# Kernel optimization log

Measured on AMD Instinct MI355X. Metric: run time of the kernel, lower is better.

Reference implementation:

```python
import jax, jax.numpy as jnp
import numpy as np
import math

D_MODEL = 1024
N_HEADS = 16
D_K = D_MODEL // N_HEADS
B, S = 2, 2048


def setup_inputs() -> dict:
    key = jax.random.key(0)
    ks = jax.random.split(key, 11)
    sc = 1.0 / math.sqrt(D_MODEL)
    inp = {
        'q': jax.random.normal(ks[0], (B, S, D_MODEL), jnp.float32),
        'k': jax.random.normal(ks[1], (B, S, D_MODEL), jnp.float32),
        'v': jax.random.normal(ks[2], (B, S, D_MODEL), jnp.float32),
        'mask': jnp.tril(jnp.ones((S, S), jnp.int32))[None, None],  # [1,1,S,S] causal
        'W_q': jax.random.normal(ks[3], (D_MODEL, D_MODEL), jnp.float32) * sc,
        'b_q': jnp.zeros((D_MODEL,), jnp.float32),
        'W_k': jax.random.normal(ks[4], (D_MODEL, D_MODEL), jnp.float32) * sc,
        'b_k': jnp.zeros((D_MODEL,), jnp.float32),
        'W_v': jax.random.normal(ks[5], (D_MODEL, D_MODEL), jnp.float32) * sc,
        'b_v': jnp.zeros((D_MODEL,), jnp.float32),
        'W_o': jax.random.normal(ks[6], (D_MODEL, D_MODEL), jnp.float32) * sc,
        'b_o': jnp.zeros((D_MODEL,), jnp.float32),
    }
    return inp


def reference(q, k, v, mask, W_q, b_q, W_k, b_k, W_v, b_v, W_o, b_o):
    # Linear projections then split heads: [B,S,D] -> [B,H,S,d_k]
    def split_heads(x):
        b, s, _ = x.shape
        return x.reshape(b, s, N_HEADS, D_K).transpose(0, 2, 1, 3)

    Q = split_heads(q @ W_q + b_q)
    K = split_heads(k @ W_k + b_k)
    V = split_heads(v @ W_v + b_v)

    scores = jnp.einsum('bhqd,bhkd->bhqk', Q, K) / math.sqrt(D_K)
    scores = jnp.where(mask == 0, jnp.float32(-1e9), scores)
    attn = jax.nn.softmax(scores, axis=-1)  # dropout is identity in eval mode
    out = jnp.einsum('bhqk,bhkd->bhqd', attn, V)
    out = out.transpose(0, 2, 1, 3).reshape(q.shape[0], -1, D_MODEL)
    return out @ W_o + b_o
```

## Files before the change

kernel.cpp:

```cpp
#include <hip/hip_runtime.h>
#include <hip/hip_bf16.h>

#define D_MODEL 1024
#define S_LEN   2048
#define BATCH   2
#define NH      16
#define DK      64

typedef __bf16 bf16_t;
typedef __attribute__((ext_vector_type(8))) __bf16 bf16x8;
typedef __attribute__((ext_vector_type(4))) float f32x4;

#if __has_builtin(__builtin_amdgcn_exp2f)
#define EXP2F(x) __builtin_amdgcn_exp2f(x)
#else
#define EXP2F(x) exp2f(x)
#endif

#define Q_SCALE 0.1803368801111204f

#define GLDS16(gp, lp) __builtin_amdgcn_global_load_lds( \
    (const __attribute__((address_space(1))) void*)(gp), \
    (__attribute__((address_space(3))) void*)(lp), 16, 0, 0)

__global__ __launch_bounds__(256) void cvt_qkv(const float* __restrict__ q,
                                               const float* __restrict__ k,
                                               const float* __restrict__ v,
                                               bf16_t* __restrict__ out) {
    const long NELEM = (long)BATCH * S_LEN * D_MODEL;
    const float* src = (blockIdx.y == 0) ? q : (blockIdx.y == 1) ? k : v;
    long i = ((long)blockIdx.x * 256 + threadIdx.x) * 8;
    float4 a = *(const float4*)(src + i);
    float4 b = *(const float4*)(src + i + 4);
    bf16x8 o;
    o[0] = (bf16_t)a.x; o[1] = (bf16_t)a.y; o[2] = (bf16_t)a.z; o[3] = (bf16_t)a.w;
    o[4] = (bf16_t)b.x; o[5] = (bf16_t)b.y; o[6] = (bf16_t)b.z; o[7] = (bf16_t)b.w;
    *(bf16x8*)(out + blockIdx.y * NELEM + i) = o;
}

__global__ void wt_transpose4(const float* __restrict__ Wq, const float* __restrict__ Wk,
                              const float* __restrict__ Wv, const float* __restrict__ Wo,
                              bf16_t* __restrict__ WqkvT, bf16_t* __restrict__ WoT) {
    __shared__ float t[32][33];
    const float* in = (blockIdx.z == 0) ? Wq : (blockIdx.z == 1) ? Wk
                    : (blockIdx.z == 2) ? Wv : Wo;
    bf16_t* out = (blockIdx.z < 3) ? (WqkvT + (long)blockIdx.z * D_MODEL * D_MODEL) : WoT;
    int tx = threadIdx.x, ty = threadIdx.y;
    int gx = blockIdx.x * 32, gy = blockIdx.y * 32;
#pragma unroll
    for (int i = 0; i < 32; i += 8)
        t[ty + i][tx] = in[(gy + ty + i) * D_MODEL + gx + tx];
    __syncthreads();
#pragma unroll
    for (int i = 0; i < 32; i += 8)
        out[(gx + ty + i) * D_MODEL + gy + tx] = (bf16_t)t[tx][ty + i];
}

__global__ void v_transpose(const bf16_t* __restrict__ in, bf16_t* __restrict__ out) {
    __shared__ bf16_t t[32][33];
    int tx = threadIdx.x, ty = threadIdx.y;
    int bh = blockIdx.z;
    int s0 = blockIdx.x * 32, d0 = blockIdx.y * 32;
    const bf16_t* ip = in + (long)bh * S_LEN * DK;
    bf16_t* op = out + (long)bh * DK * S_LEN;
#pragma unroll
    for (int i = 0; i < 32; i += 8)
        t[ty + i][tx] = ip[(long)(s0 + ty + i) * DK + d0 + tx];
    __syncthreads();
#pragma unroll
    for (int i = 0; i < 32; i += 8)
        op[(long)(d0 + ty + i) * S_LEN + s0 + tx] = t[tx][ty + i];
}

#define BM 128
#define BN 128
#define BKT 64

__device__ __forceinline__ void swizzle_xy(int bx, int by, int& n0, int& m0) {
    int lin = by * 8 + bx;
    n0 = (lin >> 5) * BN;
    m0 = (lin & 31) * BM;
}

__device__ __forceinline__ void stage_swz(const bf16_t* __restrict__ G, int row0,
                                          int k0, bf16_t* __restrict__ Ls, int tid) {
#pragma unroll
    for (int it = 0; it < 4; ++it) {
        int g = it * 256 + tid;
        int row = g >> 3;
        int c = (g & 7) ^ (row & 7);
        GLDS16(&G[(long)(row0 + row) * D_MODEL + k0 + c * 8],
               &Ls[(it * 256 + (tid & ~63)) * 8]);
    }
}

__device__ __forceinline__ bf16x8 frag_swz(const bf16_t* __restrict__ Ls, int row, int cg) {
    return *(const bf16x8*)(&Ls[(row * 8 + (cg ^ (row & 7))) * 8]);
}

__global__ __launch_bounds__(256) void gemm_qkv(
    const bf16_t* __restrict__ qkvb, const bf16_t* __restrict__ WqkvT,
    const float* __restrict__ bq, const float* __restrict__ bk, const float* __restrict__ bv,
    bf16_t* __restrict__ Qw, bf16_t* __restrict__ Kw, bf16_t* __restrict__ Vw)
{
    __shared__ __align__(16) bf16_t As[BM * BKT];
    __shared__ __align__(16) bf16_t Bs[BN * BKT];
    const int z = blockIdx.z;
    const bf16_t* A  = qkvb + (long)z * BATCH * S_LEN * D_MODEL;
    const bf16_t* BT = WqkvT + (long)z * D_MODEL * D_MODEL;
    const float* bias = (z == 0) ? bq : (z == 1) ? bk : bv;
    bf16_t* Cb = (z == 0) ? Qw : (z == 1) ? Kw : Vw;
    const float oscale = (z == 0) ? Q_SCALE : 1.0f;

    const int tid  = threadIdx.x;
    const int wave = tid >> 6, lane = tid & 63;
    const int lrow = lane & 15, kgrp = lane >> 4;
    const int wm = (wave >> 1) * 64, wn = (wave & 1) * 64;
    int m0, n0;
    swizzle_xy(blockIdx.x, blockIdx.y, n0, m0);

    f32x4 acc[4][4] = {};

    for (int k0 = 0; k0 < D_MODEL; k0 += BKT) {
        stage_swz(A, m0, k0, As, tid);
        stage_swz(BT, n0, k0, Bs, tid);
        __syncthreads();
#pragma unroll
        for (int kk = 0; kk < 2; ++kk) {
            bf16x8 af[4], bfr[4];
#pragma unroll
            for (int mi = 0; mi < 4; ++mi)
                af[mi] = frag_swz(As, wm + mi * 16 + lrow, kk * 4 + kgrp);
#pragma unroll
            for (int ni = 0; ni < 4; ++ni)
                bfr[ni] = frag_swz(Bs, wn + ni * 16 + lrow, kk * 4 + kgrp);
#pragma unroll
            for (int mi = 0; mi < 4; ++mi)
#pragma unroll
                for (int ni = 0; ni < 4; ++ni)
                    acc[mi][ni] = __builtin_amdgcn_mfma_f32_16x16x32_bf16(af[mi], bfr[ni], acc[mi][ni], 0, 0, 0);
        }
        __syncthreads();
    }

#pragma unroll
    for (int mi = 0; mi < 4; ++mi)
#pragma unroll
        for (int ni = 0; ni < 4; ++ni) {
            int col = n0 + wn + ni * 16 + lrow;
            float bvf = bias[col];
#pragma unroll
            for (int r = 0; r < 4; ++r) {
                int row = m0 + wm + mi * 16 + kgrp * 4 + r;
                float vv = (acc[mi][ni][r] + bvf) * oscale;
                int b = row >> 11, s = row & (S_LEN - 1);
                int h = col >> 6, d = col & (DK - 1);
                Cb[(((long)(b * NH + h) * S_LEN + s) * DK) + d] = (bf16_t)vv;
            }
        }
}

__global__ __launch_bounds__(256) void gemm_out(
    const bf16_t* __restrict__ A, const bf16_t* __restrict__ BT,
    const float* __restrict__ bias, float* __restrict__ Cf)
{
    __shared__ __align__(16) bf16_t As[BM * BKT];
    __shared__ __align__(16) bf16_t Bs[BN * BKT];
    const int tid  = threadIdx.x;
    const int wave = tid >> 6, lane = tid & 63;
    const int lrow = lane & 15, kgrp = lane >> 4;
    const int wm = (wave >> 1) * 64, wn = (wave & 1) * 64;
    int m0, n0;
    swizzle_xy(blockIdx.x, blockIdx.y, n0, m0);

    f32x4 acc[4][4] = {};

    for (int k0 = 0; k0 < D_MODEL; k0 += BKT) {
        stage_swz(A, m0, k0, As, tid);
        stage_swz(BT, n0, k0, Bs, tid);
        __syncthreads();
#pragma unroll
        for (int kk = 0; kk < 2; ++kk) {
            bf16x8 af[4], bfr[4];
#pragma unroll
            for (int mi = 0; mi < 4; ++mi)
                af[mi] = frag_swz(As, wm + mi * 16 + lrow, kk * 4 + kgrp);
#pragma unroll
            for (int ni = 0; ni < 4; ++ni)
                bfr[ni] = frag_swz(Bs, wn + ni * 16 + lrow, kk * 4 + kgrp);
#pragma unroll
            for (int mi = 0; mi < 4; ++mi)
#pragma unroll
                for (int ni = 0; ni < 4; ++ni)
                    acc[mi][ni] = __builtin_amdgcn_mfma_f32_16x16x32_bf16(af[mi], bfr[ni], acc[mi][ni], 0, 0, 0);
        }
        __syncthreads();
    }

#pragma unroll
    for (int mi = 0; mi < 4; ++mi)
#pragma unroll
        for (int ni = 0; ni < 4; ++ni) {
            int col = n0 + wn + ni * 16 + lrow;
            float bvf = bias[col];
#pragma unroll
            for (int r = 0; r < 4; ++r) {
                int row = m0 + wm + mi * 16 + kgrp * 4 + r;
                Cf[(long)row * D_MODEL + col] = acc[mi][ni][r] + bvf;
            }
        }
}

__global__ __launch_bounds__(256, 5) void attn_kernel(
    const bf16_t* __restrict__ Q, const bf16_t* __restrict__ K,
    const bf16_t* __restrict__ Vt, bf16_t* __restrict__ O)
{
    __shared__ __align__(16) bf16_t Ks[64 * 72];
    __shared__ __align__(16) bf16_t Vs[64 * 72];
    __shared__ __align__(16) bf16_t Ps[4][16 * 72];

    const int bh = blockIdx.y;
    const int qi = gridDim.x - 1 - blockIdx.x;
    const int q0 = qi * 64;
    const int tid = threadIdx.x, wave = tid >> 6, lane = tid & 63;
    const int lrow = lane & 15, kgrp = lane >> 4;
    const int qrow = q0 + wave * 16;

    const bf16_t* Qh  = Q  + (long)bh * S_LEN * DK;
    const bf16_t* Kh  = K  + (long)bh * S_LEN * DK;
    const bf16_t* Vth = Vt + (long)bh * DK * S_LEN;

    const int f0 = tid * 8;
    const int r0 = f0 >> 6, c0 = f0 & 63;
    const int r1 = (f0 + 2048) >> 6;

    bf16x8 qf[2];
#pragma unroll
    for (int kk = 0; kk < 2; ++kk)
        qf[kk] = *(const bf16x8*)(&Qh[(qrow + lrow) * DK + kk * 32 + kgrp * 8]);

    f32x4 acc[4] = {};
    float lsum[4] = {0.f, 0.f, 0.f, 0.f};

    const int nt = qi + 1;

    uint4 kpre0 = *(const uint4*)(&Kh[(long)r0 * DK + c0]);
    uint4 kpre1 = *(const uint4*)(&Kh[(long)r1 * DK + c0]);
    uint4 vpre0 = *(const uint4*)(&Vth[(long)r0 * S_LEN + c0]);
    uint4 vpre1 = *(const uint4*)(&Vth[(long)r1 * S_LEN + c0]);

    for (int t = 0; t < nt; ++t) {
        __syncthreads();
        *(uint4*)(&Ks[r0 * 72 + c0]) = kpre0;
        *(uint4*)(&Ks[r1 * 72 + c0]) = kpre1;
        *(uint4*)(&Vs[r0 * 72 + c0]) = vpre0;
        *(uint4*)(&Vs[r1 * 72 + c0]) = vpre1;
        if (t + 1 < nt) {
            const int j0n = (t + 1) * 64;
            kpre0 = *(const uint4*)(&Kh[(long)(j0n + r0) * DK + c0]);
            kpre1 = *(const uint4*)(&Kh[(long)(j0n + r1) * DK + c0]);
            vpre0 = *(const uint4*)(&Vth[(long)r0 * S_LEN + j0n + c0]);
            vpre1 = *(const uint4*)(&Vth[(long)r1 * S_LEN + j0n + c0]);
        }
        __syncthreads();

        const int j0 = t * 64;

        f32x4 sc[4] = {};
#pragma unroll
        for (int kk = 0; kk < 2; ++kk)
#pragma unroll
            for (int ni = 0; ni < 4; ++ni) {
                bf16x8 kf = *(const bf16x8*)(&Ks[(ni * 16 + lrow) * 72 + kk * 32 + kgrp * 8]);
                sc[ni] = __builtin_amdgcn_mfma_f32_16x16x32_bf16(qf[kk], kf, sc[ni], 0, 0, 0);
            }

        const bool needmask = (j0 + 63 > qrow);
        if (needmask) {
#pragma unroll
            for (int r = 0; r < 4; ++r) {
                int row = qrow + kgrp * 4 + r;
#pragma unroll
                for (int ni = 0; ni < 4; ++ni) {
                    int colj = j0 + ni * 16 + lrow;
                    float pv = EXP2F(sc[ni][r]);
                    if (colj > row) pv = 0.f;
                    lsum[r] += pv;
                    Ps[wave][(kgrp * 4 + r) * 72 + ni * 16 + lrow] = (bf16_t)pv;
                }
            }
        } else {
#pragma unroll
            for (int r = 0; r < 4; ++r)
#pragma unroll
                for (int ni = 0; ni < 4; ++ni) {
                    float pv = EXP2F(sc[ni][r]);
                    lsum[r] += pv;
                    Ps[wave][(kgrp * 4 + r) * 72 + ni * 16 + lrow] = (bf16_t)pv;
                }
        }

#pragma unroll
        for (int kk = 0; kk < 2; ++kk) {
            bf16x8 pf = *(const bf16x8*)(&Ps[wave][lrow * 72 + kk * 32 + kgrp * 8]);
#pragma unroll
            for (int di = 0; di < 4; ++di) {
                bf16x8 vf = *(const bf16x8*)(&Vs[(di * 16 + lrow) * 72 + kk * 32 + kgrp * 8]);
                acc[di] = __builtin_amdgcn_mfma_f32_16x16x32_bf16(pf, vf, acc[di], 0, 0, 0);
            }
        }
    }

#pragma unroll
    for (int r = 0; r < 4; ++r)
#pragma unroll
        for (int off = 1; off < 16; off <<= 1)
            lsum[r] += __shfl_xor(lsum[r], off);

    const int b = bh >> 4, h = bh & (NH - 1);
#pragma unroll
    for (int r = 0; r < 4; ++r) {
        int s = qrow + kgrp * 4 + r;
        float inv = 1.f / lsum[r];
#pragma unroll
        for (int di = 0; di < 4; ++di) {
            int d = di * 16 + lrow;
            O[((long)(b * S_LEN + s)) * D_MODEL + h * DK + d] = (bf16_t)(acc[di][r] * inv);
        }
    }
}

extern "C" void kernel_launch(void* const* d_in, const int* in_sizes, int n_in,
                              void* d_out, int out_size, void* d_ws, size_t ws_size,
                              hipStream_t stream) {
    const float* q  = (const float*)d_in[0];
    const float* k  = (const float*)d_in[1];
    const float* v  = (const float*)d_in[2];
    const float* Wq = (const float*)d_in[4];
    const float* bq = (const float*)d_in[5];
    const float* Wk = (const float*)d_in[6];
    const float* bk = (const float*)d_in[7];
    const float* Wv = (const float*)d_in[8];
    const float* bv = (const float*)d_in[9];
    const float* Wo = (const float*)d_in[10];
    const float* bo = (const float*)d_in[11];

    char* ws = (char*)d_ws;
    const size_t Mi = 1024 * 1024;
    bf16_t* WqkvT = (bf16_t*)(ws);
    bf16_t* WoT   = (bf16_t*)(ws + 6 * Mi);
    bf16_t* Qw    = (bf16_t*)(ws + 8 * Mi);
    bf16_t* Kw    = (bf16_t*)(ws + 16 * Mi);
    bf16_t* Vw    = (bf16_t*)(ws + 24 * Mi);
    bf16_t* qkvb  = (bf16_t*)(ws + 32 * Mi);
    bf16_t* Vtw   = (bf16_t*)(ws + 32 * Mi);
    bf16_t* Aw    = (bf16_t*)(ws + 40 * Mi);

    const long NELEM = (long)BATCH * S_LEN * D_MODEL;
    cvt_qkv<<<dim3((int)(NELEM / 2048), 3), 256, 0, stream>>>(q, k, v, qkvb);

    dim3 tb(32, 8);
    wt_transpose4<<<dim3(D_MODEL / 32, D_MODEL / 32, 4), tb, 0, stream>>>(
        Wq, Wk, Wv, Wo, WqkvT, WoT);

    gemm_qkv<<<dim3(D_MODEL / BN, (BATCH * S_LEN) / BM, 3), 256, 0, stream>>>(
        qkvb, WqkvT, bq, bk, bv, Qw, Kw, Vw);

    v_transpose<<<dim3(S_LEN / 32, DK / 32, BATCH * NH), tb, 0, stream>>>(Vw, Vtw);

    attn_kernel<<<dim3(S_LEN / 64, BATCH * NH), 256, 0, stream>>>(Qw, Kw, Vtw, Aw);

    gemm_out<<<dim3(D_MODEL / BN, (BATCH * S_LEN) / BM), 256, 0, stream>>>(
        Aw, WoT, bo, (float*)d_out);
}
```

Baseline: 264.2 us.

## Split causal attention over key chunks with atomic fp32 accumulation

```diff
diff --git a/kernel.cpp b/kernel.cpp
--- a/kernel.cpp
+++ b/kernel.cpp
@@ -211,16 +211,30 @@
         }
 }
 
+__global__ __launch_bounds__(256) void zero_acc(float* __restrict__ Oacc,
+                                                float* __restrict__ Lacc) {
+    f32x4 z = {0.f, 0.f, 0.f, 0.f};
+    int b = blockIdx.x;
+    if (b < 4096)
+        *(f32x4*)(&Oacc[((long)b * 256 + threadIdx.x) * 4]) = z;
+    else
+        *(f32x4*)(&Lacc[((long)(b - 4096) * 256 + threadIdx.x) * 4]) = z;
+}
+
 __global__ __launch_bounds__(256, 5) void attn_kernel(
     const bf16_t* __restrict__ Q, const bf16_t* __restrict__ K,
-    const bf16_t* __restrict__ Vt, bf16_t* __restrict__ O)
+    const bf16_t* __restrict__ Vt, float* __restrict__ Oacc,
+    float* __restrict__ Lacc)
 {
+    const int ci = blockIdx.x, qi = blockIdx.y, bh = blockIdx.z;
+    const int t0 = ci * 8;
+    if (t0 > qi) return;
+    const int t1 = min(t0 + 8, qi + 1);
+
     __shared__ __align__(16) bf16_t Ks[64 * 72];
     __shared__ __align__(16) bf16_t Vs[64 * 72];
     __shared__ __align__(16) bf16_t Ps[4][16 * 72];
 
-    const int bh = blockIdx.y;
-    const int qi = gridDim.x - 1 - blockIdx.x;
     const int q0 = qi * 64;
     const int tid = threadIdx.x, wave = tid >> 6, lane = tid & 63;
     const int lrow = lane & 15, kgrp = lane >> 4;
@@ -242,20 +256,19 @@
     f32x4 acc[4] = {};
     float lsum[4] = {0.f, 0.f, 0.f, 0.f};
 
-    const int nt = qi + 1;
-
-    uint4 kpre0 = *(const uint4*)(&Kh[(long)r0 * DK + c0]);
-    uint4 kpre1 = *(const uint4*)(&Kh[(long)r1 * DK + c0]);
-    uint4 vpre0 = *(const uint4*)(&Vth[(long)r0 * S_LEN + c0]);
-    uint4 vpre1 = *(const uint4*)(&Vth[(long)r1 * S_LEN + c0]);
-
-    for (int t = 0; t < nt; ++t) {
+    const int j00 = t0 * 64;
+    uint4 kpre0 = *(const uint4*)(&Kh[(long)(j00 + r0) * DK + c0]);
+    uint4 kpre1 = *(const uint4*)(&Kh[(long)(j00 + r1) * DK + c0]);
+    uint4 vpre0 = *(const uint4*)(&Vth[(long)r0 * S_LEN + j00 + c0]);
+    uint4 vpre1 = *(const uint4*)(&Vth[(long)r1 * S_LEN + j00 + c0]);
+
+    for (int t = t0; t < t1; ++t) {
         __syncthreads();
         *(uint4*)(&Ks[r0 * 72 + c0]) = kpre0;
         *(uint4*)(&Ks[r1 * 72 + c0]) = kpre1;
         *(uint4*)(&Vs[r0 * 72 + c0]) = vpre0;
         *(uint4*)(&Vs[r1 * 72 + c0]) = vpre1;
-        if (t + 1 < nt) {
+        if (t + 1 < t1) {
             const int j0n = (t + 1) * 64;
             kpre0 = *(const uint4*)(&Kh[(long)(j0n + r0) * DK + c0]);
             kpre1 = *(const uint4*)(&Kh[(long)(j0n + r1) * DK + c0]);
@@ -317,17 +330,37 @@
         for (int off = 1; off < 16; off <<= 1)
             lsum[r] += __shfl_xor(lsum[r], off);
 
-    const int b = bh >> 4, h = bh & (NH - 1);
 #pragma unroll
     for (int r = 0; r < 4; ++r) {
-        int s = qrow + kgrp * 4 + r;
-        float inv = 1.f / lsum[r];
-#pragma unroll
-        for (int di = 0; di < 4; ++di) {
-            int d = di * 16 + lrow;
-            O[((long)(b * S_LEN + s)) * D_MODEL + h * DK + d] = (bf16_t)(acc[di][r] * inv);
-        }
+        int q = qrow + kgrp * 4 + r;
+        float* orow = &Oacc[((long)bh * S_LEN + q) * DK];
+#pragma unroll
+        for (int di = 0; di < 4; ++di)
+            unsafeAtomicAdd(&orow[di * 16 + lrow], acc[di][r]);
+        if (lrow == 0)
+            unsafeAtomicAdd(&Lacc[bh * S_LEN + q], lsum[r]);
     }
+}
+
+__global__ __launch_bounds__(256) void attn_norm(const float* __restrict__ Oacc,
+                                                 const float* __restrict__ Lacc,
+                                                 bf16_t* __restrict__ Aw) {
+    long i8 = ((long)blockIdx.x * 256 + threadIdx.x) * 8;
+    int row = (int)(i8 >> 10);
+    int col = (int)(i8 & 1023);
+    int b = row >> 11, s = row & (S_LEN - 1);
+    int h = col >> 6, d = col & (DK - 1);
+    int bh = b * NH + h;
+    float inv = 1.f / Lacc[bh * S_LEN + s];
+    const float* src = &Oacc[((long)bh * S_LEN + s) * DK + d];
+    float4 a = *(const float4*)src;
+    float4 c = *(const float4*)(src + 4);
+    bf16x8 o;
+    o[0] = (bf16_t)(a.x * inv); o[1] = (bf16_t)(a.y * inv);
+    o[2] = (bf16_t)(a.z * inv); o[3] = (bf16_t)(a.w * inv);
+    o[4] = (bf16_t)(c.x * inv); o[5] = (bf16_t)(c.y * inv);
+    o[6] = (bf16_t)(c.z * inv); o[7] = (bf16_t)(c.w * inv);
+    *(bf16x8*)(&Aw[i8]) = o;
 }
 
 extern "C" void kernel_launch(void* const* d_in, const int* in_sizes, int n_in,
@@ -354,7 +387,9 @@
     bf16_t* Vw    = (bf16_t*)(ws + 24 * Mi);
     bf16_t* qkvb  = (bf16_t*)(ws + 32 * Mi);
     bf16_t* Vtw   = (bf16_t*)(ws + 32 * Mi);
-    bf16_t* Aw    = (bf16_t*)(ws + 40 * Mi);
+    float*  Oacc  = (float*) (ws + 40 * Mi);
+    float*  Lacc  = (float*) (ws);
+    bf16_t* Aw    = (bf16_t*)(ws + 24 * Mi);
 
     const long NELEM = (long)BATCH * S_LEN * D_MODEL;
     cvt_qkv<<<dim3((int)(NELEM / 2048), 3), 256, 0, stream>>>(q, k, v, qkvb);
@@ -368,7 +403,12 @@
 
     v_transpose<<<dim3(S_LEN / 32, DK / 32, BATCH * NH), tb, 0, stream>>>(Vw, Vtw);
 
-    attn_kernel<<<dim3(S_LEN / 64, BATCH * NH), 256, 0, stream>>>(Qw, Kw, Vtw, Aw);
+    zero_acc<<<4160, 256, 0, stream>>>(Oacc, Lacc);
+
+    attn_kernel<<<dim3(8, S_LEN / 64, BATCH * NH), 256, 0, stream>>>(
+        Qw, Kw, Vtw, Oacc, Lacc);
+
+    attn_norm<<<(int)(NELEM / 2048), 256, 0, stream>>>(Oacc, Lacc, Aw);
 
     gemm_out<<<dim3(D_MODEL / BN, (BATCH * S_LEN) / BM), 256, 0, stream>>>(
         Aw, WoT, bo, (float*)d_out);
```

Measured after the change: 326.2 us. +23.5%, slower.

## Split attention KV loop across two wave groups with LDS reduction

Applied to the files above, without the earlier changes.

```diff
diff --git a/kernel.cpp b/kernel.cpp
--- a/kernel.cpp
+++ b/kernel.cpp
@@ -211,20 +211,22 @@
         }
 }
 
-__global__ __launch_bounds__(256, 5) void attn_kernel(
+__global__ __launch_bounds__(512, 4) void attn_kernel(
     const bf16_t* __restrict__ Q, const bf16_t* __restrict__ K,
     const bf16_t* __restrict__ Vt, bf16_t* __restrict__ O)
 {
-    __shared__ __align__(16) bf16_t Ks[64 * 72];
-    __shared__ __align__(16) bf16_t Vs[64 * 72];
-    __shared__ __align__(16) bf16_t Ps[4][16 * 72];
+    __shared__ __align__(16) bf16_t Ka[64 * 72], Va[64 * 72];
+    __shared__ __align__(16) bf16_t Kb[64 * 72], Vb[64 * 72];
+    __shared__ __align__(16) bf16_t Ps[8][16 * 72];
+    __shared__ float Ms[4 * 64 * 20];
 
     const int bh = blockIdx.y;
     const int qi = gridDim.x - 1 - blockIdx.x;
     const int q0 = qi * 64;
     const int tid = threadIdx.x, wave = tid >> 6, lane = tid & 63;
+    const int grp = wave >> 2, w4 = wave & 3;
     const int lrow = lane & 15, kgrp = lane >> 4;
-    const int qrow = q0 + wave * 16;
+    const int qrow = q0 + w4 * 16;
 
     const bf16_t* Qh  = Q  + (long)bh * S_LEN * DK;
     const bf16_t* Kh  = K  + (long)bh * S_LEN * DK;
@@ -232,7 +234,6 @@
 
     const int f0 = tid * 8;
     const int r0 = f0 >> 6, c0 = f0 & 63;
-    const int r1 = (f0 + 2048) >> 6;
 
     bf16x8 qf[2];
 #pragma unroll
@@ -243,89 +244,119 @@
     float lsum[4] = {0.f, 0.f, 0.f, 0.f};
 
     const int nt = qi + 1;
-
-    uint4 kpre0 = *(const uint4*)(&Kh[(long)r0 * DK + c0]);
-    uint4 kpre1 = *(const uint4*)(&Kh[(long)r1 * DK + c0]);
-    uint4 vpre0 = *(const uint4*)(&Vth[(long)r0 * S_LEN + c0]);
-    uint4 vpre1 = *(const uint4*)(&Vth[(long)r1 * S_LEN + c0]);
-
-    for (int t = 0; t < nt; ++t) {
-        __syncthreads();
-        *(uint4*)(&Ks[r0 * 72 + c0]) = kpre0;
-        *(uint4*)(&Ks[r1 * 72 + c0]) = kpre1;
-        *(uint4*)(&Vs[r0 * 72 + c0]) = vpre0;
-        *(uint4*)(&Vs[r1 * 72 + c0]) = vpre1;
-        if (t + 1 < nt) {
-            const int j0n = (t + 1) * 64;
-            kpre0 = *(const uint4*)(&Kh[(long)(j0n + r0) * DK + c0]);
-            kpre1 = *(const uint4*)(&Kh[(long)(j0n + r1) * DK + c0]);
-            vpre0 = *(const uint4*)(&Vth[(long)r0 * S_LEN + j0n + c0]);
-            vpre1 = *(const uint4*)(&Vth[(long)r1 * S_LEN + j0n + c0]);
-        }
-        __syncthreads();
-
-        const int j0 = t * 64;
-
-        f32x4 sc[4] = {};
-#pragma unroll
-        for (int kk = 0; kk < 2; ++kk)
-#pragma unroll
-            for (int ni = 0; ni < 4; ++ni) {
-                bf16x8 kf = *(const bf16x8*)(&Ks[(ni * 16 + lrow) * 72 + kk * 32 + kgrp * 8]);
-                sc[ni] = __builtin_amdgcn_mfma_f32_16x16x32_bf16(qf[kk], kf, sc[ni], 0, 0, 0);
+    const int nst = (nt + 1) >> 1;
+
+    int ja = 0, jb = min(1, qi) * 64;
+    uint4 kpa = *(const uint4*)(&Kh[(long)(ja + r0) * DK + c0]);
+    uint4 vpa = *(const uint4*)(&Vth[(long)r0 * S_LEN + ja + c0]);
+    uint4 kpb = *(const uint4*)(&Kh[(long)(jb + r0) * DK + c0]);
+    uint4 vpb = *(const uint4*)(&Vth[(long)r0 * S_LEN + jb + c0]);
+
+    for (int st = 0; st < nst; ++st) {
+        __syncthreads();
+        *(uint4*)(&Ka[r0 * 72 + c0]) = kpa;
+        *(uint4*)(&Va[r0 * 72 + c0]) = vpa;
+        *(uint4*)(&Kb[r0 * 72 + c0]) = kpb;
+        *(uint4*)(&Vb[r0 * 72 + c0]) = vpb;
+        if (st + 1 < nst) {
+            int ta2 = (st + 1) * 2;
+            int ja2 = ta2 * 64, jb2 = min(ta2 + 1, qi) * 64;
+            kpa = *(const uint4*)(&Kh[(long)(ja2 + r0) * DK + c0]);
+            vpa = *(const uint4*)(&Vth[(long)r0 * S_LEN + ja2 + c0]);
+            kpb = *(const uint4*)(&Kh[(long)(jb2 + r0) * DK + c0]);
+            vpb = *(const uint4*)(&Vth[(long)r0 * S_LEN + jb2 + c0]);
+        }
+        __syncthreads();
+
+        const int myt = st * 2 + grp;
+        if (myt < nt) {
+            const bf16_t* Ks = grp ? Kb : Ka;
+            const bf16_t* Vs = grp ? Vb : Va;
+            const int j0 = myt * 64;
+
+            f32x4 sc[4] = {};
+#pragma unroll
+            for (int kk = 0; kk < 2; ++kk)
+#pragma unroll
+                for (int ni = 0; ni < 4; ++ni) {
+                    bf16x8 kf = *(const bf16x8*)(&Ks[(ni * 16 + lrow) * 72 + kk * 32 + kgrp * 8]);
+                    sc[ni] = __builtin_amdgcn_mfma_f32_16x16x32_bf16(qf[kk], kf, sc[ni], 0, 0, 0);
+                }
+
+            const bool needmask = (j0 + 63 > qrow);
+            if (needmask) {
+#pragma unroll
+                for (int r = 0; r < 4; ++r) {
+                    int row = qrow + kgrp * 4 + r;
+#pragma unroll
+                    for (int ni = 0; ni < 4; ++ni) {
+                        int colj = j0 + ni * 16 + lrow;
+                        float pv = EXP2F(sc[ni][r]);
+                        if (colj > row) pv = 0.f;
+                        lsum[r] += pv;
+                        Ps[wave][(kgrp * 4 + r) * 72 + ni * 16 + lrow] = (bf16_t)pv;
+                    }
+                }
+            } else {
+#pragma unroll
+                for (int r = 0; r < 4; ++r)
+#pragma unroll
+                    for (int ni = 0; ni < 4; ++ni) {
+                        float pv = EXP2F(sc[ni][r]);
+                        lsum[r] += pv;
+                        Ps[wave][(kgrp * 4 + r) * 72 + ni * 16 + lrow] = (bf16_t)pv;
+                    }
             }
 
-        const bool needmask = (j0 + 63 > qrow);
-        if (needmask) {
-#pragma unroll
-            for (int r = 0; r < 4; ++r) {
-                int row = qrow + kgrp * 4 + r;
-#pragma unroll
-                for (int ni = 0; ni < 4; ++ni) {
-                    int colj = j0 + ni * 16 + lrow;
-                    float pv = EXP2F(sc[ni][r]);
-                    if (colj > row) pv = 0.f;
-                    lsum[r] += pv;
-                    Ps[wave][(kgrp * 4 + r) * 72 + ni * 16 + lrow] = (bf16_t)pv;
+#pragma unroll
+            for (int kk = 0; kk < 2; ++kk) {
+                bf16x8 pf = *(const bf16x8*)(&Ps[wave][lrow * 72 + kk * 32 + kgrp * 8]);
+#pragma unroll
+                for (int di = 0; di < 4; ++di) {
+                    bf16x8 vf = *(const bf16x8*)(&Vs[(di * 16 + lrow) * 72 + kk * 32 + kgrp * 8]);
+                    acc[di] = __builtin_amdgcn_mfma_f32_16x16x32_bf16(pf, vf, acc[di], 0, 0, 0);
                 }
             }
-        } else {
-#pragma unroll
-            for (int r = 0; r < 4; ++r)
-#pragma unroll
-                for (int ni = 0; ni < 4; ++ni) {
-                    float pv = EXP2F(sc[ni][r]);
-                    lsum[r] += pv;
-                    Ps[wave][(kgrp * 4 + r) * 72 + ni * 16 + lrow] = (bf16_t)pv;
-                }
-        }
-
-#pragma unroll
-        for (int kk = 0; kk < 2; ++kk) {
-            bf16x8 pf = *(const bf16x8*)(&Ps[wave][lrow * 72 + kk * 32 + kgrp * 8]);
+        }
+    }
+
+    if (grp == 1) {
+        float* ms = &Ms[(w4 * 64 + lane) * 20];
+#pragma unroll
+        for (int r = 0; r < 4; ++r) {
+#pragma unroll
+            for (int di = 0; di < 4; ++di)
+                ms[r * 4 + di] = acc[di][r];
+            ms[16 + r] = lsum[r];
+        }
+    }
+    __syncthreads();
+    if (grp == 0) {
+        const float* ms = &Ms[(w4 * 64 + lane) * 20];
+#pragma unroll
+        for (int r = 0; r < 4; ++r) {
+#pragma unroll
+            for (int di = 0; di < 4; ++di)
+                acc[di][r] += ms[r * 4 + di];
+            lsum[r] += ms[16 + r];
+        }
+
+#pragma unroll
+        for (int r = 0; r < 4; ++r)
+#pragma unroll
+            for (int off = 1; off < 16; off <<= 1)
+                lsum[r] += __shfl_xor(lsum[r], off);
+
+        const int b = bh >> 4, h = bh & (NH - 1);
+#pragma unroll
+        for (int r = 0; r < 4; ++r) {
+            int s = qrow + kgrp * 4 + r;
+            float inv = 1.f / lsum[r];
 #pragma unroll
             for (int di = 0; di < 4; ++di) {
-                bf16x8 vf = *(const bf16x8*)(&Vs[(di * 16 + lrow) * 72 + kk * 32 + kgrp * 8]);
-                acc[di] = __builtin_amdgcn_mfma_f32_16x16x32_bf16(pf, vf, acc[di], 0, 0, 0);
+                int d = di * 16 + lrow;
+                O[((long)(b * S_LEN + s)) * D_MODEL + h * DK + d] = (bf16_t)(acc[di][r] * inv);
             }
-        }
-    }
-
-#pragma unroll
-    for (int r = 0; r < 4; ++r)
-#pragma unroll
-        for (int off = 1; off < 16; off <<= 1)
-            lsum[r] += __shfl_xor(lsum[r], off);
-
-    const int b = bh >> 4, h = bh & (NH - 1);
-#pragma unroll
-    for (int r = 0; r < 4; ++r) {
-        int s = qrow + kgrp * 4 + r;
-        float inv = 1.f / lsum[r];
-#pragma unroll
-        for (int di = 0; di < 4; ++di) {
-            int d = di * 16 + lrow;
-            O[((long)(b * S_LEN + s)) * D_MODEL + h * DK + d] = (bf16_t)(acc[di][r] * inv);
         }
     }
 }
@@ -354,7 +385,7 @@
     bf16_t* Vw    = (bf16_t*)(ws + 24 * Mi);
     bf16_t* qkvb  = (bf16_t*)(ws + 32 * Mi);
     bf16_t* Vtw   = (bf16_t*)(ws + 32 * Mi);
-    bf16_t* Aw    = (bf16_t*)(ws + 40 * Mi);
+    bf16_t* Aw    = (bf16_t*)(ws + 24 * Mi);
 
     const long NELEM = (long)BATCH * S_LEN * D_MODEL;
     cvt_qkv<<<dim3((int)(NELEM / 2048), 3), 256, 0, stream>>>(q, k, v, qkvb);
@@ -368,7 +399,7 @@
 
     v_transpose<<<dim3(S_LEN / 32, DK / 32, BATCH * NH), tb, 0, stream>>>(Vw, Vtw);
 
-    attn_kernel<<<dim3(S_LEN / 64, BATCH * NH), 256, 0, stream>>>(Qw, Kw, Vtw, Aw);
+    attn_kernel<<<dim3(S_LEN / 64, BATCH * NH), 512, 0, stream>>>(Qw, Kw, Vtw, Aw);
 
     gemm_out<<<dim3(D_MODEL / BN, (BATCH * S_LEN) / BM), 256, 0, stream>>>(
         Aw, WoT, bo, (float*)d_out);
```

Result: no change. 262.9 us (-0.5%).

## Load V fragments directly from global and swizzle P tile in LDS

Applied to the files above, without the earlier changes.

```diff
diff --git a/kernel.cpp b/kernel.cpp
--- a/kernel.cpp
+++ b/kernel.cpp
@@ -216,7 +216,6 @@
     const bf16_t* __restrict__ Vt, bf16_t* __restrict__ O)
 {
     __shared__ __align__(16) bf16_t Ks[64 * 72];
-    __shared__ __align__(16) bf16_t Vs[64 * 72];
     __shared__ __align__(16) bf16_t Ps[4][16 * 72];
 
     const int bh = blockIdx.y;
@@ -246,25 +245,29 @@
 
     uint4 kpre0 = *(const uint4*)(&Kh[(long)r0 * DK + c0]);
     uint4 kpre1 = *(const uint4*)(&Kh[(long)r1 * DK + c0]);
-    uint4 vpre0 = *(const uint4*)(&Vth[(long)r0 * S_LEN + c0]);
-    uint4 vpre1 = *(const uint4*)(&Vth[(long)r1 * S_LEN + c0]);
+
+    const int pg_rd0 = ((0 * 4 + kgrp) + 2 * (lrow >> 2)) & 7;
+    const int pg_rd1 = ((1 * 4 + kgrp) + 2 * (lrow >> 2)) & 7;
 
     for (int t = 0; t < nt; ++t) {
         __syncthreads();
         *(uint4*)(&Ks[r0 * 72 + c0]) = kpre0;
         *(uint4*)(&Ks[r1 * 72 + c0]) = kpre1;
-        *(uint4*)(&Vs[r0 * 72 + c0]) = vpre0;
-        *(uint4*)(&Vs[r1 * 72 + c0]) = vpre1;
         if (t + 1 < nt) {
             const int j0n = (t + 1) * 64;
             kpre0 = *(const uint4*)(&Kh[(long)(j0n + r0) * DK + c0]);
             kpre1 = *(const uint4*)(&Kh[(long)(j0n + r1) * DK + c0]);
-            vpre0 = *(const uint4*)(&Vth[(long)r0 * S_LEN + j0n + c0]);
-            vpre1 = *(const uint4*)(&Vth[(long)r1 * S_LEN + j0n + c0]);
         }
         __syncthreads();
 
         const int j0 = t * 64;
+
+        bf16x8 vf[2][4];
+#pragma unroll
+        for (int kk = 0; kk < 2; ++kk)
+#pragma unroll
+            for (int di = 0; di < 4; ++di)
+                vf[kk][di] = *(const bf16x8*)(&Vth[(long)(di * 16 + lrow) * S_LEN + j0 + kk * 32 + kgrp * 8]);
 
         f32x4 sc[4] = {};
 #pragma unroll
@@ -276,38 +279,32 @@
             }
 
         const bool needmask = (j0 + 63 > qrow);
-        if (needmask) {
-#pragma unroll
-            for (int r = 0; r < 4; ++r) {
-                int row = qrow + kgrp * 4 + r;
-#pragma unroll
-                for (int ni = 0; ni < 4; ++ni) {
+#pragma unroll
+        for (int r = 0; r < 4; ++r) {
+            const int prow = kgrp * 4 + r;
+            const int row = qrow + prow;
+#pragma unroll
+            for (int ni = 0; ni < 4; ++ni) {
+                float pv = EXP2F(sc[ni][r]);
+                if (needmask) {
                     int colj = j0 + ni * 16 + lrow;
-                    float pv = EXP2F(sc[ni][r]);
                     if (colj > row) pv = 0.f;
-                    lsum[r] += pv;
-                    Ps[wave][(kgrp * 4 + r) * 72 + ni * 16 + lrow] = (bf16_t)pv;
                 }
+                lsum[r] += pv;
+                const int pg = ((ni * 2 + (lrow >> 3)) + 2 * kgrp) & 7;
+                Ps[wave][prow * 72 + pg * 8 + (lrow & 7)] = (bf16_t)pv;
             }
-        } else {
-#pragma unroll
-            for (int r = 0; r < 4; ++r)
-#pragma unroll
-                for (int ni = 0; ni < 4; ++ni) {
-                    float pv = EXP2F(sc[ni][r]);
-                    lsum[r] += pv;
-                    Ps[wave][(kgrp * 4 + r) * 72 + ni * 16 + lrow] = (bf16_t)pv;
-                }
-        }
-
-#pragma unroll
-        for (int kk = 0; kk < 2; ++kk) {
-            bf16x8 pf = *(const bf16x8*)(&Ps[wave][lrow * 72 + kk * 32 + kgrp * 8]);
-#pragma unroll
-            for (int di = 0; di < 4; ++di) {
-                bf16x8 vf = *(const bf16x8*)(&Vs[(di * 16 + lrow) * 72 + kk * 32 + kgrp * 8]);
-                acc[di] = __builtin_amdgcn_mfma_f32_16x16x32_bf16(pf, vf, acc[di], 0, 0, 0);
-            }
+        }
+
+        {
+            bf16x8 pf0 = *(const bf16x8*)(&Ps[wave][lrow * 72 + pg_rd0 * 8]);
+#pragma unroll
+            for (int di = 0; di < 4; ++di)
+                acc[di] = __builtin_amdgcn_mfma_f32_16x16x32_bf16(pf0, vf[0][di], acc[di], 0, 0, 0);
+            bf16x8 pf1 = *(const bf16x8*)(&Ps[wave][lrow * 72 + pg_rd1 * 8]);
+#pragma unroll
+            for (int di = 0; di < 4; ++di)
+                acc[di] = __builtin_amdgcn_mfma_f32_16x16x32_bf16(pf1, vf[1][di], acc[di], 0, 0, 0);
         }
     }
 
@@ -354,7 +351,7 @@
     bf16_t* Vw    = (bf16_t*)(ws + 24 * Mi);
     bf16_t* qkvb  = (bf16_t*)(ws + 32 * Mi);
     bf16_t* Vtw   = (bf16_t*)(ws + 32 * Mi);
-    bf16_t* Aw    = (bf16_t*)(ws + 40 * Mi);
+    bf16_t* Aw    = (bf16_t*)(ws + 24 * Mi);
 
     const long NELEM = (long)BATCH * S_LEN * D_MODEL;
     cvt_qkv<<<dim3((int)(NELEM / 2048), 3), 256, 0, stream>>>(q, k, v, qkvb);
```

Result: slower. 345.6 us (+30.8%).
